# Kernel tuning notes

Measured on AMD Instinct MI355X. Metric: run time of the kernel, lower is better.

Reference implementation:

```python
import jax, jax.numpy as jnp
import numpy as np

N = 100000   # nodes
E = 1600000  # edges
G = 64       # graphs in batch
DIMS = [(7, 128), (128, 128), (128, 256)]
EPS = 1e-5


def setup_inputs() -> dict:
    key = jax.random.key(0)
    ks = jax.random.split(key, 32)
    inp = {}
    inp["x"] = jax.random.normal(ks[0], (N, 7), dtype=jnp.float32)
    inp["edge_index"] = jax.random.randint(ks[1], (2, E), 0, N, dtype=jnp.int64)
    inp["batch"] = jnp.sort(jax.random.randint(ks[2], (N,), 0, G, dtype=jnp.int64))
    ki = 3
    for i, (din, dout) in enumerate(DIMS):
        inp[f"Wl{i}"] = jax.random.normal(ks[ki], (din, dout), dtype=jnp.float32) * 0.05; ki += 1
        inp[f"bl{i}"] = jnp.zeros((dout,), dtype=jnp.float32)
        inp[f"Wr{i}"] = jax.random.normal(ks[ki], (din, dout), dtype=jnp.float32) * 0.05; ki += 1
        inp[f"g{i}"] = jax.random.uniform(ks[ki], (dout,), dtype=jnp.float32) + 0.5; ki += 1
        inp[f"be{i}"] = jax.random.normal(ks[ki], (dout,), dtype=jnp.float32) * 0.1; ki += 1
        inp[f"rm{i}"] = jax.random.normal(ks[ki], (dout,), dtype=jnp.float32) * 0.1; ki += 1
        inp[f"rv{i}"] = jax.random.uniform(ks[ki], (dout,), dtype=jnp.float32) + 0.5; ki += 1
    return inp


def _sage(x, src, dst, Wl, bl, Wr):
    # mean-aggregate neighbor features: out[i] = mean_{(j->i)} x[j]
    agg = jax.ops.segment_sum(x[src], dst, num_segments=N)          # [N, din]
    cnt = jax.ops.segment_sum(jnp.ones((src.shape[0],), x.dtype), dst, num_segments=N)
    mean = agg / jnp.maximum(cnt, 1.0)[:, None]
    return x @ Wl + bl + mean @ Wr


def _bn_relu(x, g, be, rm, rv):
    # BatchNorm1d in eval mode (running stats) + ReLU; dropout is a no-op in eval
    return jax.nn.relu((x - rm) * jax.lax.rsqrt(rv + EPS) * g + be)


def reference(x, edge_index, batch,
              Wl0, bl0, Wr0, g0, be0, rm0, rv0,
              Wl1, bl1, Wr1, g1, be1, rm1, rv1,
              Wl2, bl2, Wr2, g2, be2, rm2, rv2):
    src, dst = edge_index[0], edge_index[1]
    layers = [(Wl0, bl0, Wr0, g0, be0, rm0, rv0),
              (Wl1, bl1, Wr1, g1, be1, rm1, rv1),
              (Wl2, bl2, Wr2, g2, be2, rm2, rv2)]
    for Wl, bl, Wr, g, be, rm, rv in layers:
        x = _sage(x, src, dst, Wl, bl, Wr)
        x = _bn_relu(x, g, be, rm, rv)
    pooled = jax.ops.segment_sum(x, batch, num_segments=G)  # global_add_pool
    return (pooled, x)
```

## Files before the change

### kernel.cpp

```cpp
#include <hip/hip_runtime.h>
#include <hip/hip_bf16.h>

#define EPSV 1e-5f
#define PSHIFT 6
#define PMASK 63
#define PCAP 1536
#define B1SHIFT 11
#define B1MASK ((1 << B1SHIFT) - 1)
#define B1CAP 34816
#define SPLIT 16

typedef __attribute__((ext_vector_type(8))) short bf16x8;
typedef __attribute__((ext_vector_type(4))) float f32x4;

__device__ __forceinline__ float bf2f(unsigned short u) {
    unsigned x = ((unsigned)u) << 16;
    return __builtin_bit_cast(float, x);
}
__device__ __forceinline__ unsigned short f2bf(float f) {
    unsigned x = __builtin_bit_cast(unsigned, f);
    unsigned r = (x + 0x7fffu + ((x >> 16) & 1u)) >> 16;
    return (unsigned short)r;
}


__global__ __launch_bounds__(256) void k_scatter1(const int* __restrict__ src,
                                                  const int* __restrict__ dst,
                                                  int* __restrict__ bcnt1,
                                                  unsigned* __restrict__ stg1,
                                                  int E, int NB1) {
    __shared__ int hist[64], sbase[64], scur[64];
    int t = threadIdx.x;
    int base = blockIdx.x * 2048;
    if (t < 64) { hist[t] = 0; scur[t] = 0; }
    __syncthreads();
    unsigned val[8];
    int cb[8];
#pragma unroll
    for (int k = 0; k < 8; k++) {
        int i = base + k * 256 + t;
        if (i < E) {
            int d = __builtin_nontemporal_load(&dst[i]);
            int s = __builtin_nontemporal_load(&src[i]);
            cb[k] = d >> B1SHIFT;
            val[k] = ((unsigned)s << B1SHIFT) | (unsigned)(d & B1MASK);
            atomicAdd(&hist[cb[k]], 1);
        } else
            cb[k] = -1;
    }
    __syncthreads();
    if (t < NB1 && hist[t] > 0) sbase[t] = atomicAdd(&bcnt1[t], hist[t]);
    __syncthreads();
#pragma unroll
    for (int k = 0; k < 8; k++) {
        if (cb[k] >= 0) {
            int r = atomicAdd(&scur[cb[k]], 1);
            int slot = sbase[cb[k]] + r;
            if (slot < B1CAP) stg1[(size_t)cb[k] * B1CAP + slot] = val[k];
        }
    }
}

__global__ __launch_bounds__(256) void k_scatter2(const int* __restrict__ bcnt1,
                                                  const unsigned* __restrict__ stg1,
                                                  int* __restrict__ pcnt,
                                                  unsigned* __restrict__ pstg) {
    __shared__ int hist[32], sbase[32], scur[32];
    int cb = blockIdx.x >> 4;
    int sl = blockIdx.x & (SPLIT - 1);
    int t = threadIdx.x;
    if (t < 32) { hist[t] = 0; scur[t] = 0; }
    int cnt = min(bcnt1[cb], B1CAP);
    int per = (cnt + SPLIT - 1) / SPLIT;
    int lo = sl * per, hi = min(lo + per, cnt);
    __syncthreads();
    const unsigned* sp = stg1 + (size_t)cb * B1CAP;
    for (int j = lo + t; j < hi; j += 256)
        atomicAdd(&hist[(sp[j] >> 6) & 31], 1);
    __syncthreads();
    if (t < 32 && hist[t] > 0) sbase[t] = atomicAdd(&pcnt[(cb << 5) + t], hist[t]);
    __syncthreads();
    for (int j = lo + t; j < hi; j += 256) {
        unsigned v = sp[j];
        int pr = (v >> 6) & 31;
        int r = atomicAdd(&scur[pr], 1);
        int slot = sbase[pr] + r;
        if (slot < PCAP)
            pstg[(size_t)((cb << 5) + pr) * PCAP + slot] =
                ((v >> 5) & ~63u) | (v & 63u);
    }
}

__global__ __launch_bounds__(256) void k_meta(const int* __restrict__ pcnt,
                                              int* __restrict__ pbase,
                                              int* __restrict__ off,
                                              const int* __restrict__ batch,
                                              int* __restrict__ gstart,
                                              int NPART, int Nn, int G) {
    if (blockIdx.x == 1) {
        int g = threadIdx.x;
        if (g > G) return;
        if (g == G) {
            gstart[G] = Nn;
            return;
        }
        int lo = 0, hi = Nn;
        while (lo < hi) {
            int mid = (lo + hi) >> 1;
            if (batch[mid] < g) lo = mid + 1;
            else hi = mid;
        }
        gstart[g] = lo;
        return;
    }
    __shared__ int red[256];
    int t = threadIdx.x;
    int chunk = (NPART + 255) / 256;
    int lo = t * chunk, hi = min(lo + chunk, NPART);
    int s = 0;
    for (int p = lo; p < hi; p++) {
        int tt = min(pcnt[p], PCAP);
        pbase[p] = tt;
        s += tt;
    }
    red[t] = s;
    __syncthreads();
    for (int d = 1; d < 256; d <<= 1) {
        int v = (t >= d) ? red[t - d] : 0;
        __syncthreads();
        red[t] += v;
        __syncthreads();
    }
    int base = (t == 0) ? 0 : red[t - 1];
    for (int p = lo; p < hi; p++) {
        int tt = pbase[p];
        pbase[p] = base;
        base += tt;
    }
    if (t == 255) off[Nn] = red[255];
}

__global__ __launch_bounds__(256) void k_build(const int* __restrict__ pcnt,
                                               const unsigned* __restrict__ pstg,
                                               const int* __restrict__ pbase,
                                               int* __restrict__ off,
                                               int* __restrict__ csr, int Nn) {
    __shared__ unsigned ed[PCAP];
    __shared__ int srt[PCAP];
    __shared__ int cnt[64], loff[64], cur[64];
    int p = blockIdx.x, t = threadIdx.x;
    int tot = min(pcnt[p], PCAP);
    if (t < 64) cnt[t] = 0;
    __syncthreads();
    const unsigned* sp = pstg + (size_t)p * PCAP;
    for (int j = t; j < tot; j += 256) {
        unsigned e = __builtin_nontemporal_load(&sp[j]);
        ed[j] = e;
        atomicAdd(&cnt[e & PMASK], 1);
    }
    __syncthreads();
    if (t == 0) {
        int a = 0;
        for (int j = 0; j < 64; j++) {
            loff[j] = a;
            cur[j] = a;
            a += cnt[j];
        }
    }
    __syncthreads();
    int base = pbase[p];
    int node0 = p << PSHIFT;
    if (t < 64 && node0 + t < Nn) off[node0 + t] = base + loff[t];
    for (int j = t; j < tot; j += 256) {
        unsigned e = ed[j];
        int pos = atomicAdd(&cur[e & PMASK], 1);
        srt[pos] = (int)(e >> PSHIFT);
    }
    __syncthreads();
    for (int j = t; j < tot; j += 256) csr[base + j] = srt[j];
}


__global__ __launch_bounds__(256) void k_agg7(const float* __restrict__ x,
                                              const int* __restrict__ off,
                                              const int* __restrict__ csr,
                                              float* __restrict__ mean, int n) {
    int i = (blockIdx.x * 256 + threadIdx.x) >> 3;
    int r = threadIdx.x & 7;
    if (i >= n) return;
    int a = off[i], b = off[i + 1];
    float acc = 0.f;
    if (r < 7) {
        int j = a;
        for (; j + 1 < b; j += 2)
            acc += x[(size_t)csr[j] * 7 + r] + x[(size_t)csr[j + 1] * 7 + r];
        if (j < b) acc += x[(size_t)csr[j] * 7 + r];
    }
    float inv = 1.0f / (float)max(b - a, 1);
    if (r < 7) mean[(size_t)i * 7 + r] = acc * inv;
}

__global__ __launch_bounds__(256) void k_agg128(const unsigned short* __restrict__ x,
                                                const int* __restrict__ off,
                                                const int* __restrict__ csr,
                                                unsigned short* __restrict__ mean,
                                                int n) {
    int h = (blockIdx.x * 256 + threadIdx.x) >> 5;
    int sl = threadIdx.x & 31;
    if (h >= n) return;
    int a = off[h], b = off[h + 1];
    float a0 = 0.f, a1 = 0.f, a2 = 0.f, a3 = 0.f;
    int j = a;
    for (; j + 3 < b; j += 4) {
        int s0 = csr[j], s1 = csr[j + 1], s2 = csr[j + 2], s3 = csr[j + 3];
        ushort4 v0 = *(const ushort4*)&x[(size_t)s0 * 128 + sl * 4];
        ushort4 v1 = *(const ushort4*)&x[(size_t)s1 * 128 + sl * 4];
        ushort4 v2 = *(const ushort4*)&x[(size_t)s2 * 128 + sl * 4];
        ushort4 v3 = *(const ushort4*)&x[(size_t)s3 * 128 + sl * 4];
        a0 += bf2f(v0.x) + bf2f(v1.x) + bf2f(v2.x) + bf2f(v3.x);
        a1 += bf2f(v0.y) + bf2f(v1.y) + bf2f(v2.y) + bf2f(v3.y);
        a2 += bf2f(v0.z) + bf2f(v1.z) + bf2f(v2.z) + bf2f(v3.z);
        a3 += bf2f(v0.w) + bf2f(v1.w) + bf2f(v2.w) + bf2f(v3.w);
    }
    for (; j < b; j++) {
        ushort4 v = *(const ushort4*)&x[(size_t)csr[j] * 128 + sl * 4];
        a0 += bf2f(v.x);
        a1 += bf2f(v.y);
        a2 += bf2f(v.z);
        a3 += bf2f(v.w);
    }
    float inv = 1.0f / (float)max(b - a, 1);
    ushort4 o;
    o.x = f2bf(a0 * inv);
    o.y = f2bf(a1 * inv);
    o.z = f2bf(a2 * inv);
    o.w = f2bf(a3 * inv);
    *(ushort4*)&mean[(size_t)h * 128 + sl * 4] = o;
}


__global__ __launch_bounds__(256) void k_prepw_all(
    const float* __restrict__ Wl1, const float* __restrict__ Wr1,
    const float* __restrict__ Wl2, const float* __restrict__ Wr2,
    unsigned short* __restrict__ Wlt1, unsigned short* __restrict__ Wrt1,
    unsigned short* __restrict__ Wlt2, unsigned short* __restrict__ Wrt2) {
    int u = blockIdx.x * 256 + threadIdx.x;
    const float* W;
    unsigned short* Wt;
    int Ncols, v;
    if (u < 32768) {
        v = u & 16383;
        W = (u < 16384) ? Wl1 : Wr1;
        Wt = (u < 16384) ? Wlt1 : Wrt1;
        Ncols = 128;
    } else {
        v = (u - 32768) & 32767;
        W = (u < 65536) ? Wl2 : Wr2;
        Wt = (u < 65536) ? Wlt2 : Wrt2;
        Ncols = 256;
    }
    int n = v % Ncols, k = v / Ncols;
    Wt[(size_t)n * 128 + k] = f2bf(W[(size_t)k * Ncols + n]);
}


__global__ __launch_bounds__(256) void k_layer0(
    const float* __restrict__ x, const float* __restrict__ mean,
    const float* __restrict__ Wl, const float* __restrict__ bl,
    const float* __restrict__ Wr, const float* __restrict__ g,
    const float* __restrict__ be, const float* __restrict__ rm,
    const float* __restrict__ rv, unsigned short* __restrict__ out, int n) {
    int tid = threadIdx.x;
    int col = tid & 127;
    int r = tid >> 7;
    int row = blockIdx.x * 2 + r;
    if (row >= n) return;
    float sc = g[col] * rsqrtf(rv[col] + EPSV);
    float sh = (bl[col] - rm[col]) * sc + be[col];
    const float* xp = x + (size_t)row * 7;
    const float* mp = mean + (size_t)row * 7;
    float acc = 0.f;
#pragma unroll
    for (int k = 0; k < 7; k++) acc += xp[k] * Wl[k * 128 + col];
#pragma unroll
    for (int k = 0; k < 7; k++) acc += mp[k] * Wr[k * 128 + col];
    float h = acc * sc + sh;
    out[(size_t)row * 128 + col] = f2bf(fmaxf(h, 0.f));
}


template <int COLS, int DOUT, bool BF16OUT>
__global__ __launch_bounds__(256) void k_mfma_layer(
    const unsigned short* __restrict__ xin, const unsigned short* __restrict__ meanb,
    const unsigned short* __restrict__ Wlt, const unsigned short* __restrict__ Wrt,
    const float* __restrict__ bl, const float* __restrict__ g,
    const float* __restrict__ be, const float* __restrict__ rm,
    const float* __restrict__ rv, void* __restrict__ outv, int n) {
    __shared__ unsigned short As[64 * 40];
    __shared__ unsigned short Bs[COLS * 40];

    int tid = threadIdx.x;
    int wave = tid >> 6;
    int lane = tid & 63;
    int m = lane & 15;
    int half = lane >> 4;
    int row0 = blockIdx.x * 64;
    int colbase = blockIdx.y * COLS;

    const int NCB = COLS / 16;
    f32x4 acc[NCB] = {};

    for (int s = 0; s < 8; s++) {
        int pass = s >> 2;
        int k0 = (s & 3) * 32;
        const unsigned short* Asrc = pass ? meanb : xin;
        const unsigned short* Wt = pass ? Wrt : Wlt;

        __syncthreads();
        {
            int rr = tid >> 2;
            int ks = (tid & 3) * 8;
            int grow = row0 + rr;
            float4 v = make_float4(0.f, 0.f, 0.f, 0.f);
            if (grow < n) v = *(const float4*)&Asrc[(size_t)grow * 128 + k0 + ks];
            *(float4*)&As[rr * 40 + ks] = v;
        }
#pragma unroll
        for (int rep = 0; rep < COLS / 64; rep++) {
            int u = tid + rep * 256;
            int nn = u >> 2;
            int ks = (u & 3) * 8;
            float4 v = *(const float4*)&Wt[(size_t)(colbase + nn) * 128 + k0 + ks];
            *(float4*)&Bs[nn * 40 + ks] = v;
        }
        __syncthreads();

        bf16x8 a = *(const bf16x8*)&As[(wave * 16 + m) * 40 + half * 8];
#pragma unroll
        for (int cb = 0; cb < NCB; cb++) {
            bf16x8 b = *(const bf16x8*)&Bs[(cb * 16 + m) * 40 + half * 8];
            acc[cb] = __builtin_amdgcn_mfma_f32_16x16x32_bf16(a, b, acc[cb], 0, 0, 0);
        }
    }

    float* outf = (float*)outv;
    unsigned short* outb = (unsigned short*)outv;
#pragma unroll
    for (int cb = 0; cb < NCB; cb++) {
        int col = colbase + cb * 16 + m;
        float sc = g[col] * rsqrtf(rv[col] + EPSV);
        float sh = (bl[col] - rm[col]) * sc + be[col];
#pragma unroll
        for (int reg = 0; reg < 4; reg++) {
            int r0 = row0 + wave * 16 + half * 4 + reg;
            if (r0 < n) {
                float h = fmaxf(acc[cb][reg] * sc + sh, 0.f);
                if (BF16OUT) outb[(size_t)r0 * DOUT + col] = f2bf(h);
                else outf[(size_t)r0 * DOUT + col] = h;
            }
        }
    }
}


__global__ __launch_bounds__(256) void k_pool(const float* __restrict__ x3,
                                              const int* __restrict__ gstart,
                                              float* __restrict__ pooled, int G) {
    const int S = 16;
    int g = blockIdx.x / S;
    int s = blockIdx.x % S;
    int a = gstart[g], b = gstart[g + 1];
    int col = threadIdx.x;
    float acc = 0.f;
    for (int r = a + s; r < b; r += S) acc += x3[(size_t)r * 256 + col];
    atomicAdd(&pooled[g * 256 + col], acc);
}


extern "C" void kernel_launch(void* const* d_in, const int* in_sizes, int n_in,
                              void* d_out, int out_size, void* d_ws, size_t ws_size,
                              hipStream_t stream) {
    const float* x = (const float*)d_in[0];
    const int* ei = (const int*)d_in[1];
    const int* batch = (const int*)d_in[2];
    const int N = in_sizes[0] / 7;
    const int E = in_sizes[1] / 2;
    const int G = 64;
    const int* src = ei;
    const int* dst = ei + E;
    const int NPART = (N + PMASK) >> PSHIFT;
    const int NB1 = (N + (1 << B1SHIFT) - 1) >> B1SHIFT;

    const float* P[21];
    for (int i = 0; i < 21; i++) P[i] = (const float*)d_in[3 + i];
    const float **L0 = P, **L1 = P + 7, **L2 = P + 14;

    char* w = (char*)d_ws;
    auto carve = [&](size_t bytes) {
        void* p = (void*)w;
        w += (bytes + 255) & ~(size_t)255;
        return p;
    };
    int* cnts = (int*)carve((size_t)(64 + NPART) * 4);
    int* bcnt1 = cnts;
    int* pcnt = cnts + 64;
    unsigned* stg1 = (unsigned*)carve((size_t)NB1 * B1CAP * 4);
    unsigned* pstg = (unsigned*)carve((size_t)NPART * PCAP * 4);
    int* pbase = (int*)carve((size_t)NPART * 4);
    int* off = (int*)carve(((size_t)N + 1) * 4);
    int* gstart = (int*)carve(((size_t)G + 1) * 4);
    float* mean7 = (float*)carve((size_t)N * 7 * 4);
    unsigned short* x1 = (unsigned short*)carve((size_t)N * 128 * 2);
    unsigned short* meanb = (unsigned short*)carve((size_t)N * 128 * 2);
    unsigned short* Wlt1 = (unsigned short*)carve((size_t)128 * 128 * 2);
    unsigned short* Wrt1 = (unsigned short*)carve((size_t)128 * 128 * 2);
    unsigned short* Wlt2 = (unsigned short*)carve((size_t)128 * 256 * 2);
    unsigned short* Wrt2 = (unsigned short*)carve((size_t)128 * 256 * 2);
    int* csr = (int*)stg1;

    float* pooled = (float*)d_out;
    float* x3 = (float*)d_out + (size_t)G * 256;

    hipMemsetAsync(cnts, 0, (size_t)(64 + NPART) * 4, stream);
    hipMemsetAsync(pooled, 0, (size_t)G * 256 * 4, stream);

    k_scatter1<<<(E + 2047) / 2048, 256, 0, stream>>>(src, dst, bcnt1, stg1, E, NB1);
    k_scatter2<<<NB1 * SPLIT, 256, 0, stream>>>(bcnt1, stg1, pcnt, pstg);
    k_meta<<<2, 256, 0, stream>>>(pcnt, pbase, off, batch, gstart, NPART, N, G);
    k_build<<<NPART, 256, 0, stream>>>(pcnt, pstg, pbase, off, csr, N);
    k_prepw_all<<<(98304 + 255) / 256, 256, 0, stream>>>(L1[0], L1[2], L2[0], L2[2],
                                                         Wlt1, Wrt1, Wlt2, Wrt2);

    k_agg7<<<(N * 8 + 255) / 256, 256, 0, stream>>>(x, off, csr, mean7, N);
    k_layer0<<<(N + 1) / 2, 256, 0, stream>>>(x, mean7, L0[0], L0[1], L0[2], L0[3],
                                              L0[4], L0[5], L0[6], x1, N);

    k_agg128<<<(N + 7) / 8, 256, 0, stream>>>(x1, off, csr, meanb, N);
    k_mfma_layer<128, 128, true><<<dim3((N + 63) / 64, 1), 256, 0, stream>>>(
        x1, meanb, Wlt1, Wrt1, L1[1], L1[3], L1[4], L1[5], L1[6], x1, N);

    k_agg128<<<(N + 7) / 8, 256, 0, stream>>>(x1, off, csr, meanb, N);
    k_mfma_layer<128, 256, false><<<dim3((N + 63) / 64, 2), 256, 0, stream>>>(
        x1, meanb, Wlt2, Wrt2, L2[1], L2[3], L2[4], L2[5], L2[6], x3, N);

    k_pool<<<G * 16, 256, 0, stream>>>(x3, gstart, pooled, G);
}
```

Baseline: 483.5 us.

## Fuse global add-pool into last MFMA layer and widen agg128 loads

The separate pooling kernel is removed. The last MFMA layer epilogue now accumulates per-graph column sums: it reduces through LDS and issues one atomic per column when the whole 64-row tile belongs to a single graph, and falls back to per-element atomics otherwise. Separately, the 128-dim aggregation uses 16 lanes per node with 16-byte loads that unpack bf16 pairs, and writes results with nontemporal stores. This saves one read pass over the 256-wide fp32 output and one launch, at the cost of atomic contention on pooled and an extra __syncthreads in the epilogue.

```diff
diff --git a/kernel.cpp b/kernel.cpp
--- a/kernel.cpp
+++ b/kernel.cpp
@@ -12,6 +12,7 @@
 
 typedef __attribute__((ext_vector_type(8))) short bf16x8;
 typedef __attribute__((ext_vector_type(4))) float f32x4;
+typedef __attribute__((ext_vector_type(4))) unsigned u32x4;
 
 __device__ __forceinline__ float bf2f(unsigned short u) {
     unsigned x = ((unsigned)u) << 16;
@@ -21,6 +22,22 @@
     unsigned x = __builtin_bit_cast(unsigned, f);
     unsigned r = (x + 0x7fffu + ((x >> 16) & 1u)) >> 16;
     return (unsigned short)r;
+}
+__device__ __forceinline__ f32x4 bflo4(u32x4 v) {
+    f32x4 r;
+    r.x = __builtin_bit_cast(float, v.x << 16);
+    r.y = __builtin_bit_cast(float, v.y << 16);
+    r.z = __builtin_bit_cast(float, v.z << 16);
+    r.w = __builtin_bit_cast(float, v.w << 16);
+    return r;
+}
+__device__ __forceinline__ f32x4 bfhi4(u32x4 v) {
+    f32x4 r;
+    r.x = __builtin_bit_cast(float, v.x & 0xffff0000u);
+    r.y = __builtin_bit_cast(float, v.y & 0xffff0000u);
+    r.z = __builtin_bit_cast(float, v.z & 0xffff0000u);
+    r.w = __builtin_bit_cast(float, v.w & 0xffff0000u);
+    return r;
 }
 
 
@@ -205,37 +222,34 @@
                                                 const int* __restrict__ csr,
                                                 unsigned short* __restrict__ mean,
                                                 int n) {
-    int h = (blockIdx.x * 256 + threadIdx.x) >> 5;
-    int sl = threadIdx.x & 31;
-    if (h >= n) return;
-    int a = off[h], b = off[h + 1];
-    float a0 = 0.f, a1 = 0.f, a2 = 0.f, a3 = 0.f;
+    int q = (blockIdx.x * 256 + threadIdx.x) >> 4;
+    int sl = threadIdx.x & 15;
+    if (q >= n) return;
+    int a = off[q], b = off[q + 1];
+    const u32x4* xr = (const u32x4*)x;
+    f32x4 aL = {0.f, 0.f, 0.f, 0.f}, aH = {0.f, 0.f, 0.f, 0.f};
     int j = a;
     for (; j + 3 < b; j += 4) {
         int s0 = csr[j], s1 = csr[j + 1], s2 = csr[j + 2], s3 = csr[j + 3];
-        ushort4 v0 = *(const ushort4*)&x[(size_t)s0 * 128 + sl * 4];
-        ushort4 v1 = *(const ushort4*)&x[(size_t)s1 * 128 + sl * 4];
-        ushort4 v2 = *(const ushort4*)&x[(size_t)s2 * 128 + sl * 4];
-        ushort4 v3 = *(const ushort4*)&x[(size_t)s3 * 128 + sl * 4];
-        a0 += bf2f(v0.x) + bf2f(v1.x) + bf2f(v2.x) + bf2f(v3.x);
-        a1 += bf2f(v0.y) + bf2f(v1.y) + bf2f(v2.y) + bf2f(v3.y);
-        a2 += bf2f(v0.z) + bf2f(v1.z) + bf2f(v2.z) + bf2f(v3.z);
-        a3 += bf2f(v0.w) + bf2f(v1.w) + bf2f(v2.w) + bf2f(v3.w);
+        u32x4 v0 = xr[(size_t)s0 * 16 + sl];
+        u32x4 v1 = xr[(size_t)s1 * 16 + sl];
+        u32x4 v2 = xr[(size_t)s2 * 16 + sl];
+        u32x4 v3 = xr[(size_t)s3 * 16 + sl];
+        aL += bflo4(v0) + bflo4(v1) + bflo4(v2) + bflo4(v3);
+        aH += bfhi4(v0) + bfhi4(v1) + bfhi4(v2) + bfhi4(v3);
     }
     for (; j < b; j++) {
-        ushort4 v = *(const ushort4*)&x[(size_t)csr[j] * 128 + sl * 4];
-        a0 += bf2f(v.x);
-        a1 += bf2f(v.y);
-        a2 += bf2f(v.z);
-        a3 += bf2f(v.w);
+        u32x4 v = xr[(size_t)csr[j] * 16 + sl];
+        aL += bflo4(v);
+        aH += bfhi4(v);
     }
     float inv = 1.0f / (float)max(b - a, 1);
-    ushort4 o;
-    o.x = f2bf(a0 * inv);
-    o.y = f2bf(a1 * inv);
-    o.z = f2bf(a2 * inv);
-    o.w = f2bf(a3 * inv);
-    *(ushort4*)&mean[(size_t)h * 128 + sl * 4] = o;
+    u32x4 o;
+    o.x = (unsigned)f2bf(aL.x * inv) | ((unsigned)f2bf(aH.x * inv) << 16);
+    o.y = (unsigned)f2bf(aL.y * inv) | ((unsigned)f2bf(aH.y * inv) << 16);
+    o.z = (unsigned)f2bf(aL.z * inv) | ((unsigned)f2bf(aH.z * inv) << 16);
+    o.w = (unsigned)f2bf(aL.w * inv) | ((unsigned)f2bf(aH.w * inv) << 16);
+    __builtin_nontemporal_store(o, (u32x4*)mean + (size_t)q * 16 + sl);
 }
 
 
@@ -295,9 +309,11 @@
     const unsigned short* __restrict__ Wlt, const unsigned short* __restrict__ Wrt,
     const float* __restrict__ bl, const float* __restrict__ g,
     const float* __restrict__ be, const float* __restrict__ rm,
-    const float* __restrict__ rv, void* __restrict__ outv, int n) {
+    const float* __restrict__ rv, void* __restrict__ outv,
+    const int* __restrict__ batchp, float* __restrict__ pooled, int n) {
     __shared__ unsigned short As[64 * 40];
     __shared__ unsigned short Bs[COLS * 40];
+    __shared__ float plds[COLS];
 
     int tid = threadIdx.x;
     int wave = tid >> 6;
@@ -306,6 +322,8 @@
     int half = lane >> 4;
     int row0 = blockIdx.x * 64;
     int colbase = blockIdx.y * COLS;
+
+    if (!BF16OUT && tid < COLS) plds[tid] = 0.f;
 
     const int NCB = COLS / 16;
     f32x4 acc[NCB] = {};
@@ -343,8 +361,20 @@
         }
     }
 
+    bool uni = true;
+    int gmin = 0;
+    if (!BF16OUT) {
+        int last = min(row0 + 63, n - 1);
+        gmin = batchp[row0];
+        uni = (gmin == batchp[last]);
+    }
+
     float* outf = (float*)outv;
     unsigned short* outb = (unsigned short*)outv;
+    float colsum[NCB];
+#pragma unroll
+    for (int cb = 0; cb < NCB; cb++) colsum[cb] = 0.f;
+
 #pragma unroll
     for (int cb = 0; cb < NCB; cb++) {
         int col = colbase + cb * 16 + m;
@@ -355,25 +385,26 @@
             int r0 = row0 + wave * 16 + half * 4 + reg;
             if (r0 < n) {
                 float h = fmaxf(acc[cb][reg] * sc + sh, 0.f);
-                if (BF16OUT) outb[(size_t)r0 * DOUT + col] = f2bf(h);
-                else outf[(size_t)r0 * DOUT + col] = h;
+                if (BF16OUT) {
+                    outb[(size_t)r0 * DOUT + col] = f2bf(h);
+                } else {
+                    outf[(size_t)r0 * DOUT + col] = h;
+                    if (uni) colsum[cb] += h;
+                    else atomicAdd(&pooled[(size_t)batchp[r0] * 256 + col], h);
+                }
             }
         }
     }
-}
-
-
-__global__ __launch_bounds__(256) void k_pool(const float* __restrict__ x3,
-                                              const int* __restrict__ gstart,
-                                              float* __restrict__ pooled, int G) {
-    const int S = 16;
-    int g = blockIdx.x / S;
-    int s = blockIdx.x % S;
-    int a = gstart[g], b = gstart[g + 1];
-    int col = threadIdx.x;
-    float acc = 0.f;
-    for (int r = a + s; r < b; r += S) acc += x3[(size_t)r * 256 + col];
-    atomicAdd(&pooled[g * 256 + col], acc);
+
+    if (!BF16OUT) {
+        if (uni) {
+#pragma unroll
+            for (int cb = 0; cb < NCB; cb++) atomicAdd(&plds[cb * 16 + m], colsum[cb]);
+            __syncthreads();
+            if (tid < COLS)
+                atomicAdd(&pooled[(size_t)gmin * 256 + colbase + tid], plds[tid]);
+        }
+    }
 }
 
 
@@ -435,13 +466,13 @@
     k_layer0<<<(N + 1) / 2, 256, 0, stream>>>(x, mean7, L0[0], L0[1], L0[2], L0[3],
                                               L0[4], L0[5], L0[6], x1, N);
 
-    k_agg128<<<(N + 7) / 8, 256, 0, stream>>>(x1, off, csr, meanb, N);
+    k_agg128<<<((size_t)N * 16 + 255) / 256, 256, 0, stream>>>(x1, off, csr, meanb, N);
     k_mfma_layer<128, 128, true><<<dim3((N + 63) / 64, 1), 256, 0, stream>>>(
-        x1, meanb, Wlt1, Wrt1, L1[1], L1[3], L1[4], L1[5], L1[6], x1, N);
-
-    k_agg128<<<(N + 7) / 8, 256, 0, stream>>>(x1, off, csr, meanb, N);
+        x1, meanb, Wlt1, Wrt1, L1[1], L1[3], L1[4], L1[5], L1[6], x1, nullptr,
+        nullptr, N);
+
+    k_agg128<<<((size_t)N * 16 + 255) / 256, 256, 0, stream>>>(x1, off, csr, meanb, N);
     k_mfma_layer<128, 256, false><<<dim3((N + 63) / 64, 2), 256, 0, stream>>>(
-        x1, meanb, Wlt2, Wrt2, L2[1], L2[3], L2[4], L2[5], L2[6], x3, N);
-
-    k_pool<<<G * 16, 256, 0, stream>>>(x3, gstart, pooled, G);
-}
+        x1, meanb, Wlt2, Wrt2, L2[1], L2[3], L2[4], L2[5], L2[6], x3, batch,
+        pooled, N);
+}
```

New measurement: 510.6 us. 5.6% more time.
